# Optimization experiments

Measured on AMD Instinct MI355X. Metric: run time of the kernel, lower is better.

Reference implementation:

```python
import jax, jax.numpy as jnp
import numpy as np

NQ = 3          # num_qubits
K = 3           # kernel_size
STRIDE = 1
CIN = 3
COUT = 4
NW = 9          # num_weight
D = 2 ** NQ     # statevector dim = 8


def _apply_ry(psi, theta, q):
    """Apply RY(theta) on qubit q (qiskit little-endian: qubit q = bit q of index).
    psi: (..., D) real statevector (circuit is H/RY/CX only -> real amplitudes).
    theta: scalar or (...,) broadcastable with psi's batch dims."""
    Dloc = psi.shape[-1]
    hi = Dloc >> (q + 1)
    lo = 1 << q
    s = psi.reshape(psi.shape[:-1] + (hi, 2, lo))
    th = jnp.asarray(theta) * 0.5
    c = jnp.cos(th)[..., None, None]   # broadcast against (..., hi, lo)
    sn = jnp.sin(th)[..., None, None]
    a = s[..., 0, :]
    b = s[..., 1, :]
    # RY = [[cos, -sin], [sin, cos]] on the qubit-q axis
    out = jnp.stack((c * a - sn * b, sn * a + c * b), axis=-2)
    return out.reshape(psi.shape)


def _apply_cx(psi, ctrl, tgt):
    """CNOT: flip bit tgt where bit ctrl is 1 (pure index permutation, real state)."""
    Dloc = psi.shape[-1]
    idx = jnp.arange(Dloc)
    perm = idx ^ (((idx >> ctrl) & 1) << tgt)
    return psi[..., perm]


def _extract_patches(X, nH, nW):
    # (B, C, nH, nW, K*K), patch flattened row-major to match torch reshape
    cols = []
    for dh in range(K):
        for dw in range(K):
            cols.append(X[:, :, dh:dh + (nH - 1) * STRIDE + 1:STRIDE,
                             dw:dw + (nW - 1) * STRIDE + 1:STRIDE])
    return jnp.stack(cols, axis=-1)


def _forward(X, W):
    B, C, H, Wd = X.shape
    # loop bound in original: range(0, H - K, STRIDE)  (note: exclusive of H-K)
    nH = (H - K + STRIDE - 1) // STRIDE
    nW = (Wd - K + STRIDE - 1) // STRIDE
    # output allocated over range(0, H, STRIDE) -> zero border remains
    nH_full = (H + STRIDE - 1) // STRIDE
    nW_full = (Wd + STRIDE - 1) // STRIDE

    patches = _extract_patches(X, nH, nW)          # (B, C, nH, nW, 9)
    onehot = jax.nn.one_hot(jnp.arange(D) % COUT, COUT, dtype=X.dtype)  # interpret: basis % COUT

    acc = jnp.zeros((B, nH, nW, COUT), X.dtype)
    for i in range(C):
        # weight part of circuit: shared across all pixels for this channel
        psi = jnp.full((D,), 1.0 / np.sqrt(D), X.dtype)   # H on every qubit from |0..0>
        for wi in range(NW):
            psi = _apply_ry(psi, W[i, wi], wi % NQ)
        for q in range(NQ - 1):
            psi = _apply_cx(psi, q, q + 1)
        # data part: vectorized over all B*nH*nW patches
        x = patches[:, i].reshape(-1, K * K)              # (N, 9)
        psi_n = jnp.broadcast_to(psi, (x.shape[0], D))
        for p in range(K * K):
            psi_n = _apply_ry(psi_n, x[:, p], p % NQ)
        for q in range(NQ - 1):
            psi_n = _apply_cx(psi_n, q, q + 1)
        probs = psi_n * psi_n                             # |amp|^2 (real state)
        acc = acc + (probs @ onehot).reshape(B, nH, nW, COUT)

    out = jnp.transpose(acc, (0, 3, 1, 2))                # (B, COUT, nH, nW)
    out = jnp.pad(out, ((0, 0), (0, 0), (0, nH_full - nH), (0, nW_full - nW)))
    return out


def setup_inputs() -> dict:
    key = jax.random.key(0)
    k1, k2 = jax.random.split(key)
    X = jax.random.uniform(k1, (32, CIN, 128, 128), jnp.float32)
    # learned rotation angles, one QNN per input channel
    W = jax.random.uniform(k2, (CIN, NW), jnp.float32) * np.float32(2.0 * np.pi)
    return {"X": X, "W": W}


def reference(X, W):
    return _forward(X, W)
```

## Files before the change

kernel.cpp:

```cpp
#include <hip/hip_runtime.h>

#define CIN   3
#define COUT  4
#define NWGT  9
#define BATCH 32
#define HDIM  128
#define WDIM  128
#define NH    125
#define NWO   125

template<int Q>
__device__ __forceinline__ void apply_ry_cs(float (&p)[8], float c, float s) {
    constexpr int lo = 1 << Q;
    #pragma unroll
    for (int i = 0; i < 8; ++i) {
        if ((i & lo) == 0) {
            float a = p[i];
            float b = p[i + lo];
            p[i]      = c * a - s * b;
            p[i + lo] = s * a + c * b;
        }
    }
}

template<int Q>
__device__ __forceinline__ void apply_ry(float (&p)[8], float ang) {
    float s, c;
    __sincosf(0.5f * ang, &s, &c);
    apply_ry_cs<Q>(p, c, s);
}

__global__ __launch_bounds__(256) void quanv_kernel(
        const float* __restrict__ X,
        const float* __restrict__ Wg,
        float* __restrict__ out) {
    __shared__ float sPsi[CIN][8];
    const int t = threadIdx.x;
    if (t < CIN) {
        const float* wr = Wg + t * NWGT;
        const float a0 = wr[0] + wr[3] + wr[6];
        const float a1 = wr[1] + wr[4] + wr[7];
        const float a2 = wr[2] + wr[5] + wr[8];
        float p[8];
        #pragma unroll
        for (int m = 0; m < 8; ++m) p[m] = 0.35355339059327373f;
        apply_ry<0>(p, a0);
        apply_ry<1>(p, a1);
        apply_ry<2>(p, a2);
        float q1[8];
        #pragma unroll
        for (int j = 0; j < 8; ++j) q1[j] = p[j ^ ((j & 1) << 1)];
        #pragma unroll
        for (int j = 0; j < 8; ++j) sPsi[t][j] = q1[j ^ (((j >> 1) & 1) << 2)];
    }
    __syncthreads();

    const int tid = blockIdx.x * blockDim.x + threadIdx.x;
    if (tid >= BATCH * HDIM * WDIM) return;
    const int w = tid % WDIM;
    const int h = (tid / WDIM) % HDIM;
    const int b = tid / (WDIM * HDIM);

    float acc[COUT] = {0.f, 0.f, 0.f, 0.f};

    if (h < NH && w < NWO) {
        #pragma unroll
        for (int c = 0; c < CIN; ++c) {
            const float* xp = X + (((size_t)b * CIN + c) * HDIM + h) * WDIM + w;
            const float s0 = xp[0] + xp[WDIM]     + xp[2 * WDIM];
            const float s1 = xp[1] + xp[WDIM + 1] + xp[2 * WDIM + 1];
            const float s2 = xp[2] + xp[WDIM + 2] + xp[2 * WDIM + 2];

            float p[8];
            #pragma unroll
            for (int m = 0; m < 8; ++m) p[m] = sPsi[c][m];
            apply_ry<0>(p, s0);
            apply_ry<1>(p, s1);
            apply_ry<2>(p, s2);

            acc[0] += p[0] * p[0] + p[4] * p[4];
            acc[3] += p[1] * p[1] + p[5] * p[5];
            acc[2] += p[2] * p[2] + p[6] * p[6];
            acc[1] += p[3] * p[3] + p[7] * p[7];
        }
    }
    float* o = out + ((size_t)b * COUT * HDIM * WDIM) + (size_t)h * WDIM + w;
    #pragma unroll
    for (int c = 0; c < COUT; ++c) o[(size_t)c * HDIM * WDIM] = acc[c];
}

extern "C" void kernel_launch(void* const* d_in, const int* in_sizes, int n_in,
                              void* d_out, int out_size, void* d_ws, size_t ws_size,
                              hipStream_t stream) {
    const float* X  = (const float*)d_in[0];
    const float* Wg = (const float*)d_in[1];
    float* out = (float*)d_out;

    const int total  = BATCH * HDIM * WDIM;
    const int block  = 256;
    const int grid   = (total + block - 1) / block;
    quanv_kernel<<<grid, block, 0, stream>>>(X, Wg, out);
}
```

Before: 11.77 us.

## Closed-form probability coefficients and 4-pixel-per-thread vectorized quanv

Precomputes per-channel quadratic-form coefficients so each pixel's class probabilities become a few FMAs of cos/sin of its column sums, instead of simulating the 8-amplitude statevector. Each thread now handles four adjacent output pixels, loading float4 rows and sharing column sums and sincos values between neighbouring windows. Output is written with float4 stores. This cuts ALU work and global load count, at the cost of a more intricate algebraic derivation that could drift numerically.

```diff
diff --git a/kernel.cpp b/kernel.cpp
--- a/kernel.cpp
+++ b/kernel.cpp
@@ -1,7 +1,6 @@
 #include <hip/hip_runtime.h>
 
 #define CIN   3
-#define COUT  4
 #define NWGT  9
 #define BATCH 32
 #define HDIM  128
@@ -10,83 +9,116 @@
 #define NWO   125
 
 template<int Q>
-__device__ __forceinline__ void apply_ry_cs(float (&p)[8], float c, float s) {
+__device__ __forceinline__ void apply_ry(float (&p)[8], float ang) {
+    float s, c;
+    __sincosf(0.5f * ang, &s, &c);
     constexpr int lo = 1 << Q;
     #pragma unroll
     for (int i = 0; i < 8; ++i) {
         if ((i & lo) == 0) {
-            float a = p[i];
-            float b = p[i + lo];
+            float a = p[i], b = p[i + lo];
             p[i]      = c * a - s * b;
             p[i + lo] = s * a + c * b;
         }
     }
 }
 
-template<int Q>
-__device__ __forceinline__ void apply_ry(float (&p)[8], float ang) {
-    float s, c;
-    __sincosf(0.5f * ang, &s, &c);
-    apply_ry_cs<Q>(p, c, s);
-}
-
 __global__ __launch_bounds__(256) void quanv_kernel(
         const float* __restrict__ X,
         const float* __restrict__ Wg,
         float* __restrict__ out) {
-    __shared__ float sPsi[CIN][8];
+    __shared__ float sC[CIN][12];
     const int t = threadIdx.x;
     if (t < CIN) {
         const float* wr = Wg + t * NWGT;
-        const float a0 = wr[0] + wr[3] + wr[6];
-        const float a1 = wr[1] + wr[4] + wr[7];
-        const float a2 = wr[2] + wr[5] + wr[8];
         float p[8];
         #pragma unroll
         for (int m = 0; m < 8; ++m) p[m] = 0.35355339059327373f;
-        apply_ry<0>(p, a0);
-        apply_ry<1>(p, a1);
-        apply_ry<2>(p, a2);
-        float q1[8];
+        apply_ry<0>(p, wr[0] + wr[3] + wr[6]);
+        apply_ry<1>(p, wr[1] + wr[4] + wr[7]);
+        apply_ry<2>(p, wr[2] + wr[5] + wr[8]);
+        float q1[8], u[8];
         #pragma unroll
         for (int j = 0; j < 8; ++j) q1[j] = p[j ^ ((j & 1) << 1)];
         #pragma unroll
-        for (int j = 0; j < 8; ++j) sPsi[t][j] = q1[j ^ (((j >> 1) & 1) << 2)];
+        for (int j = 0; j < 8; ++j) u[j] = q1[j ^ (((j >> 1) & 1) << 2)];
+
+        const float P04 = u[0]*u[0] + u[4]*u[4], P15 = u[1]*u[1] + u[5]*u[5];
+        const float P26 = u[2]*u[2] + u[6]*u[6], P37 = u[3]*u[3] + u[7]*u[7];
+        const float K1 = 0.5f*(P04 + P15), K2 = 0.5f*(P04 - P15);
+        const float K3 = -(u[0]*u[1] + u[4]*u[5]);
+        const float L1 = 0.5f*(P26 + P37), L2 = 0.5f*(P26 - P37);
+        const float L3 = -(u[2]*u[3] + u[6]*u[7]);
+        const float C02 = u[0]*u[2] + u[4]*u[6], C13 = u[1]*u[3] + u[5]*u[7];
+        const float M1 = 0.5f*(C02 + C13), M2 = 0.5f*(C02 - C13);
+        const float M3 = -0.5f*(u[0]*u[3] + u[1]*u[2] + u[4]*u[7] + u[5]*u[6]);
+        sC[t][0] = 0.5f*(K1 + L1); sC[t][1] = 0.5f*(K2 + L2); sC[t][2] = 0.5f*(K3 + L3);
+        sC[t][3] = 0.5f*(K1 - L1); sC[t][4] = 0.5f*(K2 - L2); sC[t][5] = 0.5f*(K3 - L3);
+        sC[t][6] = M1;             sC[t][7] = M2;             sC[t][8] = M3;
+        sC[t][9]  = K1 + L1;
+        sC[t][10] = K1 - L1;
+        sC[t][11] = 2.0f * M1;
     }
     __syncthreads();
 
     const int tid = blockIdx.x * blockDim.x + threadIdx.x;
-    if (tid >= BATCH * HDIM * WDIM) return;
-    const int w = tid % WDIM;
-    const int h = (tid / WDIM) % HDIM;
-    const int b = tid / (WDIM * HDIM);
+    const int w0  = (tid & 31) << 2;
+    const int row = tid >> 5;
+    const int h   = row & (HDIM - 1);
+    const int b   = row >> 7;
 
-    float acc[COUT] = {0.f, 0.f, 0.f, 0.f};
-
-    if (h < NH && w < NWO) {
+    float acc[4][4] = {{0.f}};
+    if (h < NH) {
+        const bool wfull = (w0 < 124);
         #pragma unroll
         for (int c = 0; c < CIN; ++c) {
-            const float* xp = X + (((size_t)b * CIN + c) * HDIM + h) * WDIM + w;
-            const float s0 = xp[0] + xp[WDIM]     + xp[2 * WDIM];
-            const float s1 = xp[1] + xp[WDIM + 1] + xp[2 * WDIM + 1];
-            const float s2 = xp[2] + xp[WDIM + 2] + xp[2 * WDIM + 2];
+            const float* base = X + (((size_t)b * CIN + c) << 14) + (h << 7) + w0;
+            const float4 r0 = *(const float4*)(base);
+            const float4 r1 = *(const float4*)(base + WDIM);
+            const float4 r2 = *(const float4*)(base + 2 * WDIM);
+            const float e0 = wfull ? base[4]            : 0.f;
+            const float e1 = wfull ? base[WDIM + 4]     : 0.f;
+            const float e2 = wfull ? base[2 * WDIM + 4] : 0.f;
+            float cs[5];
+            cs[0] = r0.x + r1.x + r2.x;
+            cs[1] = r0.y + r1.y + r2.y;
+            cs[2] = r0.z + r1.z + r2.z;
+            cs[3] = r0.w + r1.w + r2.w;
+            cs[4] = e0 + e1 + e2;
+            float cc[5], sn[5];
+            #pragma unroll
+            for (int j = 0; j < 5; ++j) __sincosf(cs[j], &sn[j], &cc[j]);
 
-            float p[8];
+            const float E1 = sC[c][0], E2 = sC[c][1], E3 = sC[c][2];
+            const float F1 = sC[c][3], F2 = sC[c][4], F3 = sC[c][5];
+            const float M1 = sC[c][6], M2 = sC[c][7], M3 = sC[c][8];
+            const float E1x2 = sC[c][9], F1x2 = sC[c][10], M1x2 = sC[c][11];
             #pragma unroll
-            for (int m = 0; m < 8; ++m) p[m] = sPsi[c][m];
-            apply_ry<0>(p, s0);
-            apply_ry<1>(p, s1);
-            apply_ry<2>(p, s2);
-
-            acc[0] += p[0] * p[0] + p[4] * p[4];
-            acc[3] += p[1] * p[1] + p[5] * p[5];
-            acc[2] += p[2] * p[2] + p[6] * p[6];
-            acc[1] += p[3] * p[3] + p[7] * p[7];
+            for (int j = 0; j < 4; ++j) {
+                const float cj = cc[j], sj = sn[j];
+                const float c1 = cc[j + 1], s1 = sn[j + 1];
+                const float e  = fmaf(E3, sj, fmaf(E2, cj, E1));
+                const float f  = fmaf(F3, sj, fmaf(F2, cj, F1));
+                const float g  = fmaf(M3, sj, fmaf(M2, cj, M1));
+                const float ep = E1x2 - e, fp = F1x2 - f, gp = M1x2 - g;
+                const float cls0 = fmaf(-g,  s1, fmaf(f,  c1, e));
+                const float cls2 = fmaf(2.f, e,  -cls0);
+                const float cls3 = fmaf(-gp, s1, fmaf(fp, c1, ep));
+                const float cls1 = fmaf(2.f, ep, -cls3);
+                acc[0][j] += cls0; acc[1][j] += cls1;
+                acc[2][j] += cls2; acc[3][j] += cls3;
+            }
         }
+        #pragma unroll
+        for (int j = 0; j < 4; ++j)
+            if (w0 + j >= NWO)
+                acc[0][j] = acc[1][j] = acc[2][j] = acc[3][j] = 0.f;
     }
-    float* o = out + ((size_t)b * COUT * HDIM * WDIM) + (size_t)h * WDIM + w;
+    float* ob = out + (((size_t)b * 4) << 14) + (h << 7) + w0;
     #pragma unroll
-    for (int c = 0; c < COUT; ++c) o[(size_t)c * HDIM * WDIM] = acc[c];
+    for (int k = 0; k < 4; ++k)
+        *(float4*)(ob + ((size_t)k << 14)) =
+            make_float4(acc[k][0], acc[k][1], acc[k][2], acc[k][3]);
 }
 
 extern "C" void kernel_launch(void* const* d_in, const int* in_sizes, int n_in,
@@ -96,8 +128,6 @@
     const float* Wg = (const float*)d_in[1];
     float* out = (float*)d_out;
 
-    const int total  = BATCH * HDIM * WDIM;
-    const int block  = 256;
-    const int grid   = (total + block - 1) / block;
-    quanv_kernel<<<grid, block, 0, stream>>>(X, Wg, out);
+    const int total = BATCH * HDIM * (WDIM / 4);
+    quanv_kernel<<<total / 256, 256, 0, stream>>>(X, Wg, out);
 }
```

New measurement: 10.34 us. -12.1%, faster.
